# Performance work log

Measured on AMD Instinct MI355X. Metric: run time of the kernel, lower is better.

The kernel has to match this reference:

```python
import jax, jax.numpy as jnp
import numpy as np

D_MODEL = 1024
N_HEADS = 16
D_K = D_MODEL // N_HEADS
B, S = 4, 2048


def setup_inputs() -> dict:
    key = jax.random.key(0)
    ks = jax.random.split(key, 5)
    scale = 1.0 / np.sqrt(D_MODEL)  # ~xavier scale for square matrices
    return {
        "Q": jax.random.normal(ks[0], (B, S, D_MODEL), dtype=jnp.float32),
        "length": jax.random.randint(ks[1], (B,), 1, S, dtype=jnp.int32),
        "Wq": jax.random.normal(ks[2], (D_MODEL, D_MODEL), dtype=jnp.float32) * scale,
        "bq": jnp.zeros((D_MODEL,), dtype=jnp.float32),
        "Wk": jax.random.normal(ks[3], (D_MODEL, D_MODEL), dtype=jnp.float32) * scale,
        "bk": jnp.zeros((D_MODEL,), dtype=jnp.float32),
        "Wv": jax.random.normal(ks[4], (D_MODEL, D_MODEL), dtype=jnp.float32) * scale,
        "bv": jnp.zeros((D_MODEL,), dtype=jnp.float32),
    }


def reference(Q, length, Wq, bq, Wk, bk, Wv, bv):
    b, s, d = Q.shape
    q_a = Q @ Wq + bq                                   # [b, s, d]
    # split heads: [b, h, s, d_k]
    q_s = q_a.reshape(b, s, N_HEADS, D_K).transpose(0, 2, 1, 3)
    k_s = (Q @ Wk + bk).reshape(b, s, N_HEADS, D_K).transpose(0, 2, 1, 3)
    v_s = (Q @ Wv + bv).reshape(b, s, N_HEADS, D_K).transpose(0, 2, 1, 3)

    # unnormalized exp attention with multiplicative key mask (faithful to source)
    scores = jnp.einsum("bhqd,bhkd->bhqk", q_s, k_s) / np.sqrt(D_K)
    scores = jnp.exp(scores)
    key_mask = (jnp.arange(s)[None, :] < length[:, None]).astype(scores.dtype)  # [b, k]
    scores = scores * key_mask[:, None, None, :]        # broadcast over heads, queries
    attn = scores / (jnp.sum(scores, axis=-1, keepdims=True) + 1e-8)
    context = jnp.einsum("bhqk,bhkd->bhqd", attn, v_s)
    context = context.transpose(0, 2, 1, 3).reshape(b, s, d)
    return context, q_a
```

## Files before the change

### kernel.cpp

```cpp
#include <hip/hip_runtime.h>

#define D_MODEL 1024
#define N_HEADS 16
#define D_KH    64
#define BATCH   4
#define SEQ     2048
#define M_TOTAL (BATCH*SEQ)

typedef __attribute__((ext_vector_type(8))) short short8;
typedef __attribute__((ext_vector_type(4))) float f32x4;
typedef __attribute__((ext_vector_type(4))) unsigned short u16x4;
typedef __attribute__((ext_vector_type(2))) unsigned int u32x2;

__device__ __forceinline__ unsigned short f2bf(float f) {
  union { float f; unsigned u; } v; v.f = f;
  unsigned r = v.u + 0x7FFFu + ((v.u >> 16) & 1u);
  return (unsigned short)(r >> 16);
}
__device__ __forceinline__ unsigned fbits(float f) {
  union { float f; unsigned u; } v; v.f = f; return v.u;
}

__global__ __launch_bounds__(256) void cvt_q(const float* __restrict__ Q,
                                             unsigned short* __restrict__ Qbf) {
  size_t i = (size_t)blockIdx.x * 256 + threadIdx.x;
  float4 v = ((const float4*)Q)[i];
  u16x4 o;
  o[0] = f2bf(v.x); o[1] = f2bf(v.y); o[2] = f2bf(v.z); o[3] = f2bf(v.w);
  ((u16x4*)Qbf)[i] = o;
}

__global__ __launch_bounds__(256) void cvt_wt(const float* __restrict__ Wq,
                                              const float* __restrict__ Wk,
                                              const float* __restrict__ Wv,
                                              unsigned short* __restrict__ WT) {
  const int z = blockIdx.z;
  const float* W = (z == 0) ? Wq : (z == 1) ? Wk : Wv;
  __shared__ float tile[32][33];
  const int k0 = blockIdx.y * 32, n0 = blockIdx.x * 32;
  const int tx = threadIdx.x & 31, ty = threadIdx.x >> 5;
  for (int i = 0; i < 4; ++i)
    tile[ty + i * 8][tx] = W[(size_t)(k0 + ty + i * 8) * D_MODEL + n0 + tx];
  __syncthreads();
  unsigned short* out = WT + (size_t)z * D_MODEL * D_MODEL;
  for (int i = 0; i < 4; ++i)
    out[(size_t)(n0 + ty + i * 8) * D_MODEL + k0 + tx] = f2bf(tile[tx][ty + i * 8]);
}

#define BM 128
#define BN 128
#define BK 32

__global__ __launch_bounds__(256, 2) void gemm_qkv(
    const unsigned short* __restrict__ Qbf,
    const unsigned short* __restrict__ WT,
    const float* __restrict__ bq_p, const float* __restrict__ bk_p,
    const float* __restrict__ bv_p,
    float* __restrict__ out_qa,
    unsigned short* __restrict__ kbf,
    unsigned short* __restrict__ vt) {
  const int z  = blockIdx.z;
  const int n0 = blockIdx.x * BN;
  const int m0 = blockIdx.y * BM;
  const int K  = D_MODEL;

  __shared__ unsigned short smA[BM * BK];
  __shared__ unsigned short smB[BN * BK];

  const int t    = threadIdx.x;
  const int lane = t & 63;
  const int w    = t >> 6;
  const int quad = lane >> 4;
  const int l16  = lane & 15;
  const int wr   = w >> 1, wc = w & 1;

  const unsigned short* Wz = WT + (size_t)z * D_MODEL * D_MODEL;

  f32x4 acc[4][4];
  for (int i = 0; i < 4; ++i)
    for (int j = 0; j < 4; ++j) acc[i][j] = (f32x4){0.f, 0.f, 0.f, 0.f};

  for (int k0 = 0; k0 < K; k0 += BK) {
    __syncthreads();
    for (int it = 0; it < 2; ++it) {
      int c   = t + it * 256;
      int row = c >> 2, col = (c & 3) * 8;
      const unsigned short* ga = Qbf + (size_t)(m0 + row) * K + k0 + col;
      const unsigned short* gb = Wz  + (size_t)(n0 + row) * K + k0 + col;
      __builtin_amdgcn_global_load_lds(
          (const __attribute__((address_space(1))) void*)ga,
          (__attribute__((address_space(3))) void*)&smA[c * 8], 16, 0, 0);
      __builtin_amdgcn_global_load_lds(
          (const __attribute__((address_space(1))) void*)gb,
          (__attribute__((address_space(3))) void*)&smB[c * 8], 16, 0, 0);
    }
    __syncthreads();

    short8 afr[4], bfr[4];
    for (int mi = 0; mi < 4; ++mi)
      afr[mi] = *(const short8*)&smA[(wr * 64 + mi * 16 + l16) * BK + quad * 8];
    for (int ni = 0; ni < 4; ++ni)
      bfr[ni] = *(const short8*)&smB[(wc * 64 + ni * 16 + l16) * BK + quad * 8];
    for (int mi = 0; mi < 4; ++mi)
      for (int ni = 0; ni < 4; ++ni)
        acc[mi][ni] = __builtin_amdgcn_mfma_f32_16x16x32_bf16(
            afr[mi], bfr[ni], acc[mi][ni], 0, 0, 0);
  }

  const float* bias = (z == 0) ? bq_p : (z == 1) ? bk_p : bv_p;
  if (z == 2) {
    for (int ni = 0; ni < 4; ++ni) {
      int n = n0 + wc * 64 + ni * 16 + l16;
      float bval = bias[n];
      int h = n >> 6, d = n & 63;
      for (int mi = 0; mi < 4; ++mi) {
        int m = m0 + wr * 64 + mi * 16 + quad * 4;
        int b = m >> 11, s = m & 2047;
        u16x4 o;
        for (int j = 0; j < 4; ++j) o[j] = f2bf(acc[mi][ni][j] + bval);
        *(u16x4*)&vt[(size_t)((b * 16 + h) * 64 + d) * SEQ + s] = o;
      }
    }
  } else {
    for (int ni = 0; ni < 4; ++ni) {
      int n = n0 + wc * 64 + ni * 16 + l16;
      float bval = bias[n];
      for (int mi = 0; mi < 4; ++mi) {
        int mbase = m0 + wr * 64 + mi * 16 + quad * 4;
        for (int j = 0; j < 4; ++j) {
          float v = acc[mi][ni][j] + bval;
          size_t idx = (size_t)(mbase + j) * D_MODEL + n;
          if (z == 0) out_qa[idx] = v;
          else        kbf[idx] = f2bf(v);
        }
      }
    }
  }
}

#define PST 72

__global__ __launch_bounds__(256, 2) void attn(
    const float* __restrict__ qa,
    const unsigned short* __restrict__ kbf,
    const unsigned short* __restrict__ vt,
    const int* __restrict__ length,
    float* __restrict__ ctx) {
  const int qt = blockIdx.x;
  const int bh = blockIdx.y;
  const int b = bh >> 4, h = bh & 15;
  const int len = length[b];

  const int t    = threadIdx.x;
  const int lane = t & 63;
  const int w    = t >> 6;
  const int quad = lane >> 4;
  const int l16  = lane & 15;
  const int r8   = t >> 3;
  const int c8   = (t & 7) * 8;

  __shared__ unsigned short sQ[64 * PST];
  __shared__ unsigned short sK[64 * PST];
  __shared__ unsigned short sVT[64 * PST];
  __shared__ unsigned short sP[64 * PST];

  for (int half = 0; half < 2; ++half) {
    int r = r8 + half * 32;
    const float* src = qa + (size_t)(b * SEQ + qt * 64 + r) * D_MODEL + h * D_KH + c8;
    float4 v0 = *(const float4*)src;
    float4 v1 = *(const float4*)(src + 4);
    short8 o;
    o[0] = (short)f2bf(v0.x); o[1] = (short)f2bf(v0.y);
    o[2] = (short)f2bf(v0.z); o[3] = (short)f2bf(v0.w);
    o[4] = (short)f2bf(v1.x); o[5] = (short)f2bf(v1.y);
    o[6] = (short)f2bf(v1.z); o[7] = (short)f2bf(v1.w);
    *(short8*)&sQ[r * PST + c8] = o;
  }
  __syncthreads();

  short8 qf0 = *(const short8*)&sQ[(w * 16 + l16) * PST + quad * 8];
  short8 qf1 = *(const short8*)&sQ[(w * 16 + l16) * PST + 32 + quad * 8];

  f32x4 accpv[4];
  for (int i = 0; i < 4; ++i) accpv[i] = (f32x4){0.f, 0.f, 0.f, 0.f};
  float den = 0.f;

  const float SCL = 0.125f * 1.44269504f;

  const int nkt = (len + 63) >> 6;
  for (int kt = 0; kt < nkt; ++kt) {
    __syncthreads();
    for (int half = 0; half < 2; ++half) {
      int r = r8 + half * 32;
      size_t koff = (size_t)(b * SEQ + kt * 64 + r) * D_MODEL + h * D_KH + c8;
      *(short8*)&sK[r * PST + c8] = *(const short8*)(kbf + koff);
      size_t voff = (size_t)(bh * 64 + r) * SEQ + kt * 64 + c8;
      *(short8*)&sVT[r * PST + c8] = *(const short8*)(vt + voff);
    }
    __syncthreads();

    for (int n = 0; n < 4; ++n) {
      short8 kf0 = *(const short8*)&sK[(n * 16 + l16) * PST + quad * 8];
      short8 kf1 = *(const short8*)&sK[(n * 16 + l16) * PST + 32 + quad * 8];
      f32x4 s = (f32x4){0.f, 0.f, 0.f, 0.f};
      s = __builtin_amdgcn_mfma_f32_16x16x32_bf16(kf0, qf0, s, 0, 0, 0);
      s = __builtin_amdgcn_mfma_f32_16x16x32_bf16(kf1, qf1, s, 0, 0, 0);
      int kbase = kt * 64 + n * 16 + quad * 4;
      float e0 = (kbase + 0 < len) ? exp2f(s[0] * SCL) : 0.f;
      float e1 = (kbase + 1 < len) ? exp2f(s[1] * SCL) : 0.f;
      float e2 = (kbase + 2 < len) ? exp2f(s[2] * SCL) : 0.f;
      float e3 = (kbase + 3 < len) ? exp2f(s[3] * SCL) : 0.f;
      den += (e0 + e1) + (e2 + e3);
      u32x2 pk;
      pk[0] = __builtin_amdgcn_perm(fbits(e1), fbits(e0), 0x07060302);
      pk[1] = __builtin_amdgcn_perm(fbits(e3), fbits(e2), 0x07060302);
      *(u32x2*)&sP[(w * 16 + l16) * PST + n * 16 + quad * 4] = pk;
    }

    short8 pf0 = *(const short8*)&sP[(w * 16 + l16) * PST + quad * 8];
    short8 pf1 = *(const short8*)&sP[(w * 16 + l16) * PST + 32 + quad * 8];
    for (int n2 = 0; n2 < 4; ++n2) {
      short8 vf0 = *(const short8*)&sVT[(n2 * 16 + l16) * PST + quad * 8];
      short8 vf1 = *(const short8*)&sVT[(n2 * 16 + l16) * PST + 32 + quad * 8];
      accpv[n2] = __builtin_amdgcn_mfma_f32_16x16x32_bf16(vf0, pf0, accpv[n2], 0, 0, 0);
      accpv[n2] = __builtin_amdgcn_mfma_f32_16x16x32_bf16(vf1, pf1, accpv[n2], 0, 0, 0);
    }
  }

  den += __shfl_xor(den, 16, 64);
  den += __shfl_xor(den, 32, 64);
  float inv = 1.f / (den + 1e-8f);

  {
    int q = qt * 64 + w * 16 + l16;
    float* dst = ctx + (size_t)(b * SEQ + q) * D_MODEL + h * D_KH;
    for (int n2 = 0; n2 < 4; ++n2) {
      f32x4 o = accpv[n2];
      float4 v = make_float4(o[0] * inv, o[1] * inv, o[2] * inv, o[3] * inv);
      *(float4*)(dst + n2 * 16 + quad * 4) = v;
    }
  }
}

extern "C" void kernel_launch(void* const* d_in, const int* in_sizes, int n_in,
                              void* d_out, int out_size, void* d_ws, size_t ws_size,
                              hipStream_t stream) {
  const float* Q      = (const float*)d_in[0];
  const int*   length = (const int*)d_in[1];
  const float* Wq     = (const float*)d_in[2];
  const float* bq     = (const float*)d_in[3];
  const float* Wk     = (const float*)d_in[4];
  const float* bk     = (const float*)d_in[5];
  const float* Wv     = (const float*)d_in[6];
  const float* bv     = (const float*)d_in[7];

  float* out_ctx = (float*)d_out;
  float* out_qa  = out_ctx + (size_t)M_TOTAL * D_MODEL;

  char* ws = (char*)d_ws;
  unsigned short* Qbf = (unsigned short*)ws;
  unsigned short* WT  = (unsigned short*)(ws + (size_t)16 * 1024 * 1024);
  unsigned short* Kbf = (unsigned short*)(ws + (size_t)22 * 1024 * 1024);
  unsigned short* Vt  = (unsigned short*)(ws + (size_t)38 * 1024 * 1024);

  hipLaunchKernelGGL(cvt_q, dim3((M_TOTAL * D_MODEL) / (256 * 4)), dim3(256), 0, stream,
                     Q, Qbf);
  hipLaunchKernelGGL(cvt_wt, dim3(32, 32, 3), dim3(256), 0, stream, Wq, Wk, Wv, WT);
  hipLaunchKernelGGL(gemm_qkv, dim3(D_MODEL / BN, M_TOTAL / BM, 3), dim3(256), 0, stream,
                     Qbf, WT, bq, bk, bv, out_qa, Kbf, Vt);
  hipLaunchKernelGGL(attn, dim3(SEQ / 64, BATCH * N_HEADS), dim3(256), 0, stream,
                     out_qa, Kbf, Vt, length, out_ctx);
}
```

Baseline: 261.1 us.

## Double query tile per attention block and fold softmax scale into Q

Each attention block now handles 128 queries (two 16-row groups per wave) instead of 64, so every K/V tile loaded into shared memory is reused across twice as many queries and the global K/V traffic halves. The softmax scale is folded into Q at bf16 conversion, removing a multiply per score. Fully unmasked key tiles skip the per-element length checks. The cost is more registers and shared memory per block and half as many blocks, which may reduce occupancy. Scaling Q before bf16 rounding also changes rounding slightly.

```diff
diff --git a/kernel.cpp b/kernel.cpp
--- a/kernel.cpp
+++ b/kernel.cpp
@@ -139,6 +139,7 @@
 }
 
 #define PST 72
+#define QT  128
 
 __global__ __launch_bounds__(256, 2) void attn(
     const float* __restrict__ qa,
@@ -159,83 +160,109 @@
   const int r8   = t >> 3;
   const int c8   = (t & 7) * 8;
 
-  __shared__ unsigned short sQ[64 * PST];
+  __shared__ unsigned short sQ[QT * PST];
   __shared__ unsigned short sK[64 * PST];
   __shared__ unsigned short sVT[64 * PST];
-  __shared__ unsigned short sP[64 * PST];
-
-  for (int half = 0; half < 2; ++half) {
+  __shared__ unsigned short sP[QT * PST];
+
+  const float SCL = 0.125f * 1.44269504f;
+
+  for (int half = 0; half < 4; ++half) {
     int r = r8 + half * 32;
-    const float* src = qa + (size_t)(b * SEQ + qt * 64 + r) * D_MODEL + h * D_KH + c8;
+    const float* src = qa + (size_t)(b * SEQ + qt * QT + r) * D_MODEL + h * D_KH + c8;
     float4 v0 = *(const float4*)src;
     float4 v1 = *(const float4*)(src + 4);
     short8 o;
-    o[0] = (short)f2bf(v0.x); o[1] = (short)f2bf(v0.y);
-    o[2] = (short)f2bf(v0.z); o[3] = (short)f2bf(v0.w);
-    o[4] = (short)f2bf(v1.x); o[5] = (short)f2bf(v1.y);
-    o[6] = (short)f2bf(v1.z); o[7] = (short)f2bf(v1.w);
+    o[0] = (short)f2bf(v0.x * SCL); o[1] = (short)f2bf(v0.y * SCL);
+    o[2] = (short)f2bf(v0.z * SCL); o[3] = (short)f2bf(v0.w * SCL);
+    o[4] = (short)f2bf(v1.x * SCL); o[5] = (short)f2bf(v1.y * SCL);
+    o[6] = (short)f2bf(v1.z * SCL); o[7] = (short)f2bf(v1.w * SCL);
     *(short8*)&sQ[r * PST + c8] = o;
   }
   __syncthreads();
 
-  short8 qf0 = *(const short8*)&sQ[(w * 16 + l16) * PST + quad * 8];
-  short8 qf1 = *(const short8*)&sQ[(w * 16 + l16) * PST + 32 + quad * 8];
-
-  f32x4 accpv[4];
-  for (int i = 0; i < 4; ++i) accpv[i] = (f32x4){0.f, 0.f, 0.f, 0.f};
-  float den = 0.f;
-
-  const float SCL = 0.125f * 1.44269504f;
+  short8 qf[2][2];
+  for (int g = 0; g < 2; ++g) {
+    qf[g][0] = *(const short8*)&sQ[(w * 32 + g * 16 + l16) * PST + quad * 8];
+    qf[g][1] = *(const short8*)&sQ[(w * 32 + g * 16 + l16) * PST + 32 + quad * 8];
+  }
+
+  f32x4 accpv[2][4];
+  for (int g = 0; g < 2; ++g)
+    for (int i = 0; i < 4; ++i) accpv[g][i] = (f32x4){0.f, 0.f, 0.f, 0.f};
+  float den[2] = {0.f, 0.f};
+
+  const unsigned short* kbase_p = kbf + (size_t)b * SEQ * D_MODEL + h * D_KH;
+  const unsigned short* vbase_p = vt + (size_t)bh * 64 * SEQ;
 
   const int nkt = (len + 63) >> 6;
   for (int kt = 0; kt < nkt; ++kt) {
     __syncthreads();
     for (int half = 0; half < 2; ++half) {
       int r = r8 + half * 32;
-      size_t koff = (size_t)(b * SEQ + kt * 64 + r) * D_MODEL + h * D_KH + c8;
-      *(short8*)&sK[r * PST + c8] = *(const short8*)(kbf + koff);
-      size_t voff = (size_t)(bh * 64 + r) * SEQ + kt * 64 + c8;
-      *(short8*)&sVT[r * PST + c8] = *(const short8*)(vt + voff);
+      *(short8*)&sK[r * PST + c8] =
+          *(const short8*)(kbase_p + (size_t)(kt * 64 + r) * D_MODEL + c8);
+      *(short8*)&sVT[r * PST + c8] =
+          *(const short8*)(vbase_p + (size_t)r * SEQ + kt * 64 + c8);
     }
     __syncthreads();
+
+    const bool full = ((kt + 1) << 6) <= len;
 
     for (int n = 0; n < 4; ++n) {
       short8 kf0 = *(const short8*)&sK[(n * 16 + l16) * PST + quad * 8];
       short8 kf1 = *(const short8*)&sK[(n * 16 + l16) * PST + 32 + quad * 8];
-      f32x4 s = (f32x4){0.f, 0.f, 0.f, 0.f};
-      s = __builtin_amdgcn_mfma_f32_16x16x32_bf16(kf0, qf0, s, 0, 0, 0);
-      s = __builtin_amdgcn_mfma_f32_16x16x32_bf16(kf1, qf1, s, 0, 0, 0);
-      int kbase = kt * 64 + n * 16 + quad * 4;
-      float e0 = (kbase + 0 < len) ? exp2f(s[0] * SCL) : 0.f;
-      float e1 = (kbase + 1 < len) ? exp2f(s[1] * SCL) : 0.f;
-      float e2 = (kbase + 2 < len) ? exp2f(s[2] * SCL) : 0.f;
-      float e3 = (kbase + 3 < len) ? exp2f(s[3] * SCL) : 0.f;
-      den += (e0 + e1) + (e2 + e3);
-      u32x2 pk;
-      pk[0] = __builtin_amdgcn_perm(fbits(e1), fbits(e0), 0x07060302);
-      pk[1] = __builtin_amdgcn_perm(fbits(e3), fbits(e2), 0x07060302);
-      *(u32x2*)&sP[(w * 16 + l16) * PST + n * 16 + quad * 4] = pk;
-    }
-
-    short8 pf0 = *(const short8*)&sP[(w * 16 + l16) * PST + quad * 8];
-    short8 pf1 = *(const short8*)&sP[(w * 16 + l16) * PST + 32 + quad * 8];
+      int kb = kt * 64 + n * 16 + quad * 4;
+      for (int g = 0; g < 2; ++g) {
+        f32x4 s = (f32x4){0.f, 0.f, 0.f, 0.f};
+        s = __builtin_amdgcn_mfma_f32_16x16x32_bf16(kf0, qf[g][0], s, 0, 0, 0);
+        s = __builtin_amdgcn_mfma_f32_16x16x32_bf16(kf1, qf[g][1], s, 0, 0, 0);
+        float e0, e1, e2, e3;
+        if (full) {
+          e0 = exp2f(s[0]); e1 = exp2f(s[1]);
+          e2 = exp2f(s[2]); e3 = exp2f(s[3]);
+        } else {
+          e0 = (kb + 0 < len) ? exp2f(s[0]) : 0.f;
+          e1 = (kb + 1 < len) ? exp2f(s[1]) : 0.f;
+          e2 = (kb + 2 < len) ? exp2f(s[2]) : 0.f;
+          e3 = (kb + 3 < len) ? exp2f(s[3]) : 0.f;
+        }
+        den[g] += (e0 + e1) + (e2 + e3);
+        u32x2 pk;
+        pk[0] = __builtin_amdgcn_perm(fbits(e1), fbits(e0), 0x07060302);
+        pk[1] = __builtin_amdgcn_perm(fbits(e3), fbits(e2), 0x07060302);
+        *(u32x2*)&sP[(w * 32 + g * 16 + l16) * PST + n * 16 + quad * 4] = pk;
+      }
+    }
+
+    short8 pf[2][2];
+    for (int g = 0; g < 2; ++g) {
+      pf[g][0] = *(const short8*)&sP[(w * 32 + g * 16 + l16) * PST + quad * 8];
+      pf[g][1] = *(const short8*)&sP[(w * 32 + g * 16 + l16) * PST + 32 + quad * 8];
+    }
     for (int n2 = 0; n2 < 4; ++n2) {
       short8 vf0 = *(const short8*)&sVT[(n2 * 16 + l16) * PST + quad * 8];
       short8 vf1 = *(const short8*)&sVT[(n2 * 16 + l16) * PST + 32 + quad * 8];
-      accpv[n2] = __builtin_amdgcn_mfma_f32_16x16x32_bf16(vf0, pf0, accpv[n2], 0, 0, 0);
-      accpv[n2] = __builtin_amdgcn_mfma_f32_16x16x32_bf16(vf1, pf1, accpv[n2], 0, 0, 0);
-    }
-  }
-
-  den += __shfl_xor(den, 16, 64);
-  den += __shfl_xor(den, 32, 64);
-  float inv = 1.f / (den + 1e-8f);
-
-  {
-    int q = qt * 64 + w * 16 + l16;
+      for (int g = 0; g < 2; ++g) {
+        accpv[g][n2] = __builtin_amdgcn_mfma_f32_16x16x32_bf16(vf0, pf[g][0], accpv[g][n2], 0, 0, 0);
+        accpv[g][n2] = __builtin_amdgcn_mfma_f32_16x16x32_bf16(vf1, pf[g][1], accpv[g][n2], 0, 0, 0);
+      }
+    }
+  }
+
+  for (int g = 0; g < 2; ++g) {
+    float d = den[g];
+    d += __shfl_xor(d, 16, 64);
+    d += __shfl_xor(d, 32, 64);
+    den[g] = 1.f / (d + 1e-8f);
+  }
+
+  for (int g = 0; g < 2; ++g) {
+    int q = qt * QT + w * 32 + g * 16 + l16;
     float* dst = ctx + (size_t)(b * SEQ + q) * D_MODEL + h * D_KH;
+    float inv = den[g];
     for (int n2 = 0; n2 < 4; ++n2) {
-      f32x4 o = accpv[n2];
+      f32x4 o = accpv[g][n2];
       float4 v = make_float4(o[0] * inv, o[1] * inv, o[2] * inv, o[3] * inv);
       *(float4*)(dst + n2 * 16 + quad * 4) = v;
     }
@@ -268,6 +295,6 @@
   hipLaunchKernelGGL(cvt_wt, dim3(32, 32, 3), dim3(256), 0, stream, Wq, Wk, Wv, WT);
   hipLaunchKernelGGL(gemm_qkv, dim3(D_MODEL / BN, M_TOTAL / BM, 3), dim3(256), 0, stream,
                      Qbf, WT, bq, bk, bv, out_qa, Kbf, Vt);
-  hipLaunchKernelGGL(attn, dim3(SEQ / 64, BATCH * N_HEADS), dim3(256), 0, stream,
+  hipLaunchKernelGGL(attn, dim3(SEQ / QT, BATCH * N_HEADS), dim3(256), 0, stream,
                      out_qa, Kbf, Vt, length, out_ctx);
 }
```

New measurement: 264.7 us. No clear change (+1.4%).

## Prefetch next K/V tile into registers and fold softmax scale into Q

Applied to the files above, without the earlier changes.

The attention kernel now loads the next K and V^T tile into registers while the current tile is being computed. This overlaps global-memory latency with the MFMA and exp work. The softmax scale is folded into Q before the bf16 conversion, which removes a multiply per score, and full key tiles skip the per-element mask checks. Launch bounds are raised to request 4 blocks per CU, which caps registers per thread and may cause spills given the extra prefetch registers.

```diff
diff --git a/kernel.cpp b/kernel.cpp
--- a/kernel.cpp
+++ b/kernel.cpp
@@ -140,7 +140,7 @@
 
 #define PST 72
 
-__global__ __launch_bounds__(256, 2) void attn(
+__global__ __launch_bounds__(256, 4) void attn(
     const float* __restrict__ qa,
     const unsigned short* __restrict__ kbf,
     const unsigned short* __restrict__ vt,
@@ -164,16 +164,18 @@
   __shared__ unsigned short sVT[64 * PST];
   __shared__ unsigned short sP[64 * PST];
 
+  const float SCL = 0.125f * 1.44269504f;
+
   for (int half = 0; half < 2; ++half) {
     int r = r8 + half * 32;
     const float* src = qa + (size_t)(b * SEQ + qt * 64 + r) * D_MODEL + h * D_KH + c8;
     float4 v0 = *(const float4*)src;
     float4 v1 = *(const float4*)(src + 4);
     short8 o;
-    o[0] = (short)f2bf(v0.x); o[1] = (short)f2bf(v0.y);
-    o[2] = (short)f2bf(v0.z); o[3] = (short)f2bf(v0.w);
-    o[4] = (short)f2bf(v1.x); o[5] = (short)f2bf(v1.y);
-    o[6] = (short)f2bf(v1.z); o[7] = (short)f2bf(v1.w);
+    o[0] = (short)f2bf(v0.x * SCL); o[1] = (short)f2bf(v0.y * SCL);
+    o[2] = (short)f2bf(v0.z * SCL); o[3] = (short)f2bf(v0.w * SCL);
+    o[4] = (short)f2bf(v1.x * SCL); o[5] = (short)f2bf(v1.y * SCL);
+    o[6] = (short)f2bf(v1.z * SCL); o[7] = (short)f2bf(v1.w * SCL);
     *(short8*)&sQ[r * PST + c8] = o;
   }
   __syncthreads();
@@ -185,19 +187,36 @@
   for (int i = 0; i < 4; ++i) accpv[i] = (f32x4){0.f, 0.f, 0.f, 0.f};
   float den = 0.f;
 
-  const float SCL = 0.125f * 1.44269504f;
+  const unsigned short* kbase_p = kbf + (size_t)b * SEQ * D_MODEL + h * D_KH;
+  const unsigned short* vbase_p = vt + (size_t)bh * 64 * SEQ;
 
   const int nkt = (len + 63) >> 6;
+
+  short8 rk[2], rv[2];
+  for (int half = 0; half < 2; ++half) {
+    int r = r8 + half * 32;
+    rk[half] = *(const short8*)(kbase_p + (size_t)r * D_MODEL + c8);
+    rv[half] = *(const short8*)(vbase_p + (size_t)r * SEQ + c8);
+  }
+
   for (int kt = 0; kt < nkt; ++kt) {
     __syncthreads();
     for (int half = 0; half < 2; ++half) {
       int r = r8 + half * 32;
-      size_t koff = (size_t)(b * SEQ + kt * 64 + r) * D_MODEL + h * D_KH + c8;
-      *(short8*)&sK[r * PST + c8] = *(const short8*)(kbf + koff);
-      size_t voff = (size_t)(bh * 64 + r) * SEQ + kt * 64 + c8;
-      *(short8*)&sVT[r * PST + c8] = *(const short8*)(vt + voff);
-    }
-    __syncthreads();
+      *(short8*)&sK[r * PST + c8]  = rk[half];
+      *(short8*)&sVT[r * PST + c8] = rv[half];
+    }
+    __syncthreads();
+
+    if (kt + 1 < nkt) {
+      for (int half = 0; half < 2; ++half) {
+        int r = r8 + half * 32;
+        rk[half] = *(const short8*)(kbase_p + (size_t)((kt + 1) * 64 + r) * D_MODEL + c8);
+        rv[half] = *(const short8*)(vbase_p + (size_t)r * SEQ + (kt + 1) * 64 + c8);
+      }
+    }
+
+    const bool full = ((kt + 1) << 6) <= len;
 
     for (int n = 0; n < 4; ++n) {
       short8 kf0 = *(const short8*)&sK[(n * 16 + l16) * PST + quad * 8];
@@ -205,11 +224,17 @@
       f32x4 s = (f32x4){0.f, 0.f, 0.f, 0.f};
       s = __builtin_amdgcn_mfma_f32_16x16x32_bf16(kf0, qf0, s, 0, 0, 0);
       s = __builtin_amdgcn_mfma_f32_16x16x32_bf16(kf1, qf1, s, 0, 0, 0);
-      int kbase = kt * 64 + n * 16 + quad * 4;
-      float e0 = (kbase + 0 < len) ? exp2f(s[0] * SCL) : 0.f;
-      float e1 = (kbase + 1 < len) ? exp2f(s[1] * SCL) : 0.f;
-      float e2 = (kbase + 2 < len) ? exp2f(s[2] * SCL) : 0.f;
-      float e3 = (kbase + 3 < len) ? exp2f(s[3] * SCL) : 0.f;
+      float e0, e1, e2, e3;
+      if (full) {
+        e0 = exp2f(s[0]); e1 = exp2f(s[1]);
+        e2 = exp2f(s[2]); e3 = exp2f(s[3]);
+      } else {
+        int kb = kt * 64 + n * 16 + quad * 4;
+        e0 = (kb + 0 < len) ? exp2f(s[0]) : 0.f;
+        e1 = (kb + 1 < len) ? exp2f(s[1]) : 0.f;
+        e2 = (kb + 2 < len) ? exp2f(s[2]) : 0.f;
+        e3 = (kb + 3 < len) ? exp2f(s[3]) : 0.f;
+      }
       den += (e0 + e1) + (e2 + e3);
       u32x2 pk;
       pk[0] = __builtin_amdgcn_perm(fbits(e1), fbits(e0), 0x07060302);
```

Measured after the change: 260.7 us. No clear change (-0.1%).
